# Optimization experiments

Measured on AMD Instinct MI355X. Metric: run time of the kernel, lower is better.

Reference implementation:

```python
import jax, jax.numpy as jnp
import numpy as np

N_DRUG = 20000
N_DIS = 20000
E = 300000
D_IN = 128
D_OUT = 128
W_SCALE = 0.05  # ~xavier-ish scale so leaky_relu/softmax stay well-conditioned


def setup_inputs() -> dict:
    key = jax.random.key(0)
    ks = jax.random.split(key, 17)
    f32 = jnp.float32
    inp = {
        'feat_drug': jax.random.normal(ks[0], (N_DRUG, D_IN), dtype=f32),
        'feat_disease': jax.random.normal(ks[1], (N_DIS, D_IN), dtype=f32),
        'W_ind': jax.random.normal(ks[2], (D_IN, D_OUT), dtype=f32) * W_SCALE,
        'b_ind': jax.random.normal(ks[3], (D_OUT,), dtype=f32) * W_SCALE,
        'a_ind': jax.random.normal(ks[4], (2 * D_OUT,), dtype=f32) * W_SCALE,
        'W_rev': jax.random.normal(ks[5], (D_IN, D_OUT), dtype=f32) * W_SCALE,
        'b_rev': jax.random.normal(ks[6], (D_OUT,), dtype=f32) * W_SCALE,
        'a_rev': jax.random.normal(ks[7], (2 * D_OUT,), dtype=f32) * W_SCALE,
        'W_dd': jax.random.normal(ks[8], (D_IN, D_OUT), dtype=f32) * W_SCALE,
        'b_dd': jax.random.normal(ks[9], (D_OUT,), dtype=f32) * W_SCALE,
        'a_dd': jax.random.normal(ks[10], (2 * D_OUT,), dtype=f32) * W_SCALE,
        'src_ind': jax.random.randint(ks[11], (E,), 0, N_DRUG, dtype=jnp.int32),
        'dst_ind': jax.random.randint(ks[12], (E,), 0, N_DIS, dtype=jnp.int32),
        'src_rev': jax.random.randint(ks[13], (E,), 0, N_DIS, dtype=jnp.int32),
        'dst_rev': jax.random.randint(ks[14], (E,), 0, N_DRUG, dtype=jnp.int32),
        'src_dd': jax.random.randint(ks[15], (E,), 0, N_DIS, dtype=jnp.int32),
        'dst_dd': jax.random.randint(ks[16], (E,), 0, N_DIS, dtype=jnp.int32),
    }
    return inp


def segment_softmax(e, seg, num_segments):
    # numerically stable softmax over variable-degree neighborhoods (dst segments)
    m = jax.ops.segment_max(e, seg, num_segments=num_segments)
    p = jnp.exp(e - m[seg])
    s = jax.ops.segment_sum(p, seg, num_segments=num_segments)
    return p / s[seg]


def _etype_agg(Wh_src, Wh_dst_key, a, src, dst, n_dst):
    # attn_fc(cat([Wh_src[src], Wh_dst_key[dst]])) decomposed into per-node
    # scalar projections, then gathered per edge (same math, far less traffic)
    d = Wh_src.shape[1]
    el = Wh_src @ a[:d]        # [n_src]
    er = Wh_dst_key @ a[d:]    # [n_dst]
    e = jax.nn.leaky_relu(el[src] + er[dst])          # [E], slope 0.01 as in torch
    alpha = segment_softmax(e, dst, n_dst)            # per-dst softmax (DGL mailbox)
    msg = alpha[:, None] * Wh_src[src]                # [E, d]
    return jax.ops.segment_sum(msg, dst, num_segments=n_dst)


def reference(feat_drug, feat_disease, W_ind, b_ind, a_ind, W_rev, b_rev, a_rev,
              W_dd, b_dd, a_dd, src_ind, dst_ind, src_rev, dst_rev, src_dd, dst_dd):
    # per-etype linear on source node type
    Wh_ind = feat_drug @ W_ind + b_ind       # drug nodes, etype 'indication'
    Wh_rev = feat_disease @ W_rev + b_rev    # disease nodes, etype 'rev_indication'
    Wh_dd = feat_disease @ W_dd + b_dd       # disease nodes, etype 'disease_disease'
    n_drug = feat_drug.shape[0]
    n_dis = feat_disease.shape[0]
    # etype 'indication' (drug->disease): dst key is Wh_rev_indication
    h_dis_ind = _etype_agg(Wh_ind, Wh_rev, a_ind, src_ind, dst_ind, n_dis)
    # etype 'rev_indication' (disease->drug): dst key is Wh_indication
    h_drug = _etype_agg(Wh_rev, Wh_ind, a_rev, src_rev, dst_rev, n_drug)
    # etype 'disease_disease' (homotypic): both keys Wh_dd
    h_dis_dd = _etype_agg(Wh_dd, Wh_dd, a_dd, src_dd, dst_dd, n_dis)
    # multi_update_all(..., 'sum'): sum per-etype reductions per dst node type
    h_disease = h_dis_ind + h_dis_dd
    return h_drug, h_disease
```

## Files before the change

kernel.cpp:

```cpp
#include <hip/hip_runtime.h>
#include <hip/hip_bf16.h>

typedef __hip_bfloat16 bf16;
typedef __attribute__((ext_vector_type(8))) short bf16x8;
typedef __attribute__((ext_vector_type(4))) float f32x4;

#define N_NODE 20000
#define D      128
#define NEDGE  300000
#define NROW   (3 * N_NODE)
#define NBIN   ((NROW + 255) >> 8)
#define NB3    220
#define CHUNK  4096
#define GBE    ((N_NODE + 63) / 64)
#define WT_LD  132

__device__ __forceinline__ short f2bs(float x) {
    bf16 h = __float2bfloat16(x);
    short s; __builtin_memcpy(&s, &h, 2); return s;
}

__global__ __launch_bounds__(256) void gemm_mfma_all(
    const float* __restrict__ feat_drug, const float* __restrict__ feat_dis,
    const float* __restrict__ W_ind, const float* __restrict__ b_ind,
    const float* __restrict__ a_ind,
    const float* __restrict__ W_rev, const float* __restrict__ b_rev,
    const float* __restrict__ a_rev,
    const float* __restrict__ W_dd, const float* __restrict__ b_dd,
    const float* __restrict__ a_dd,
    bf16* __restrict__ Wh_all, float* __restrict__ el_all,
    float* __restrict__ er_all) {
    __shared__ short Wt[D * WT_LD];
    const int t  = blockIdx.x / GBE;
    const int mb = blockIdx.x - t * GBE;
    const int tid = threadIdx.x;

    const float *feat, *W, *bias, *va, *vb;
    float *el_o, *er_o;
    if (t == 0)      { feat = feat_dis;  W = W_rev; bias = b_rev; va = a_rev; vb = a_ind + D; el_o = el_all;              er_o = er_all + N_NODE; }
    else if (t == 1) { feat = feat_drug; W = W_ind; bias = b_ind; va = a_ind; vb = a_rev + D; el_o = el_all + N_NODE;     er_o = er_all; }
    else             { feat = feat_dis;  W = W_dd;  bias = b_dd;  va = a_dd;  vb = a_dd + D;  el_o = el_all + 2 * N_NODE; er_o = er_all + 2 * N_NODE; }
    bf16* wh_o = Wh_all + (size_t)t * N_NODE * D;

    for (int i = tid * 4; i < D * D; i += 1024) {
        const float4 wv = *(const float4*)(W + i);
        const int k = i >> 7, n = i & (D - 1);
        Wt[(n + 0) * WT_LD + k] = f2bs(wv.x);
        Wt[(n + 1) * WT_LD + k] = f2bs(wv.y);
        Wt[(n + 2) * WT_LD + k] = f2bs(wv.z);
        Wt[(n + 3) * WT_LD + k] = f2bs(wv.w);
    }
    __syncthreads();

    const int wave = tid >> 6, lane = tid & 63;
    const int q = lane >> 4, nn = lane & 15;
    const int row0 = mb * 64 + wave * 16;
    const int arow = min(row0 + nn, N_NODE - 1);

    f32x4 acc[8];
#pragma unroll
    for (int nt = 0; nt < 8; ++nt) acc[nt] = (f32x4){0.f, 0.f, 0.f, 0.f};

#pragma unroll
    for (int ks = 0; ks < 4; ++ks) {
        const float* ap = feat + (size_t)arow * D + ks * 32 + q * 8;
        const float4 fa = *(const float4*)ap;
        const float4 fb = *(const float4*)(ap + 4);
        bf16x8 afrag;
        afrag[0] = f2bs(fa.x); afrag[1] = f2bs(fa.y);
        afrag[2] = f2bs(fa.z); afrag[3] = f2bs(fa.w);
        afrag[4] = f2bs(fb.x); afrag[5] = f2bs(fb.y);
        afrag[6] = f2bs(fb.z); afrag[7] = f2bs(fb.w);
#pragma unroll
        for (int nt = 0; nt < 8; ++nt) {
            const bf16x8 bfrag =
                *(const bf16x8*)(&Wt[(nt * 16 + nn) * WT_LD + ks * 32 + q * 8]);
            acc[nt] = __builtin_amdgcn_mfma_f32_16x16x32_bf16(afrag, bfrag,
                                                              acc[nt], 0, 0, 0);
        }
    }

    float biasv[8], vav[8], vbv[8];
#pragma unroll
    for (int nt = 0; nt < 8; ++nt) {
        const int col = nt * 16 + nn;
        biasv[nt] = bias[col]; vav[nt] = va[col]; vbv[nt] = vb[col];
    }
    float pel[4] = {0.f, 0.f, 0.f, 0.f};
    float per_[4] = {0.f, 0.f, 0.f, 0.f};
    short* whs = (short*)wh_o;
#pragma unroll
    for (int nt = 0; nt < 8; ++nt) {
#pragma unroll
        for (int r = 0; r < 4; ++r) {
            const float c = acc[nt][r] + biasv[nt];
            const int grow = row0 + q * 4 + r;
            if (grow < N_NODE)
                whs[(size_t)grow * D + nt * 16 + nn] = f2bs(c);
            pel[r] = fmaf(c, vav[nt], pel[r]);
            per_[r] = fmaf(c, vbv[nt], per_[r]);
        }
    }
#pragma unroll
    for (int r = 0; r < 4; ++r) {
#pragma unroll
        for (int mask = 1; mask < 16; mask <<= 1) {
            pel[r]  += __shfl_xor(pel[r],  mask, 64);
            per_[r] += __shfl_xor(per_[r], mask, 64);
        }
        const int grow = row0 + q * 4 + r;
        if (nn == 0 && grow < N_NODE) {
            el_o[grow] = pel[r];
            er_o[grow] = per_[r];
        }
    }
}


__global__ __launch_bounds__(256) void binct(
    const int* __restrict__ dst_rev, const int* __restrict__ dst_ind,
    const int* __restrict__ dst_dd, int* __restrict__ bin_cnt) {
    __shared__ int h[NBIN];
    const int tid = threadIdx.x;
    for (int i = tid; i < NBIN; i += 256) h[i] = 0;
    __syncthreads();
    const int base = blockIdx.x * CHUNK;
    const int lim = min(base + CHUNK, 3 * NEDGE);
    for (int i = base + tid; i < lim; i += 256) {
        const int t = (i >= 2 * NEDGE) ? 2 : (i >= NEDGE ? 1 : 0);
        const int e = i - t * NEDGE;
        const int d = (t == 0 ? dst_rev : (t == 1 ? dst_ind : dst_dd))[e];
        atomicAdd(&h[(t * N_NODE + d) >> 8], 1);
    }
    __syncthreads();
    for (int i = tid; i < NBIN; i += 256)
        if (h[i]) atomicAdd(&bin_cnt[i], h[i]);
}

__global__ __launch_bounds__(256) void binscan(
    const int* __restrict__ bin_cnt, int* __restrict__ bin_base,
    int* __restrict__ bin_cursor, int* __restrict__ row_ptr) {
    __shared__ int wsum[4];
    const int tid = threadIdx.x;
    const int lane = tid & 63, wave = tid >> 6;
    int v = (tid < NBIN) ? bin_cnt[tid] : 0;
    const int orig = v;
#pragma unroll
    for (int off = 1; off < 64; off <<= 1) {
        int t = __shfl_up(v, off, 64);
        if (lane >= off) v += t;
    }
    if (lane == 63) wsum[wave] = v;
    __syncthreads();
    if (tid == 0) {
        int a = 0;
#pragma unroll
        for (int w = 0; w < 4; ++w) { int t = wsum[w]; wsum[w] = a; a += t; }
    }
    __syncthreads();
    const int incl = wsum[wave] + v;
    const int excl = incl - orig;
    if (tid < NBIN) { bin_base[tid] = excl; bin_cursor[tid] = excl; }
    if (tid == 255) { bin_base[NBIN] = incl; row_ptr[NROW] = 3 * NEDGE; }
}

__global__ __launch_bounds__(256) void binscat(
    const int* __restrict__ src_rev, const int* __restrict__ dst_rev,
    const int* __restrict__ src_ind, const int* __restrict__ dst_ind,
    const int* __restrict__ src_dd,  const int* __restrict__ dst_dd,
    int* __restrict__ bin_cursor, unsigned* __restrict__ bin_buf) {
    __shared__ int h[NBIN];
    __shared__ int runc[NBIN];
    const int tid = threadIdx.x;
    for (int i = tid; i < NBIN; i += 256) h[i] = 0;
    __syncthreads();
    const int base = blockIdx.x * CHUNK;
    const int lim = min(base + CHUNK, 3 * NEDGE);
    for (int i = base + tid; i < lim; i += 256) {
        const int t = (i >= 2 * NEDGE) ? 2 : (i >= NEDGE ? 1 : 0);
        const int e = i - t * NEDGE;
        const int d = (t == 0 ? dst_rev : (t == 1 ? dst_ind : dst_dd))[e];
        atomicAdd(&h[(t * N_NODE + d) >> 8], 1);
    }
    __syncthreads();
    for (int i = tid; i < NBIN; i += 256)
        runc[i] = h[i] ? atomicAdd(&bin_cursor[i], h[i]) : 0;
    __syncthreads();
    for (int i = base + tid; i < lim; i += 256) {
        const int t = (i >= 2 * NEDGE) ? 2 : (i >= NEDGE ? 1 : 0);
        const int e = i - t * NEDGE;
        const int sl = (t == 0 ? src_rev : (t == 1 ? src_ind : src_dd))[e];
        const int dl = (t == 0 ? dst_rev : (t == 1 ? dst_ind : dst_dd))[e];
        const int row = t * N_NODE + dl;
        const int slot = atomicAdd(&runc[row >> 8], 1);
        bin_buf[slot] = ((unsigned)row << 16) | (unsigned)(t * N_NODE + sl);
    }
}

__global__ __launch_bounds__(256) void binsort(
    const int* __restrict__ bin_base, const unsigned* __restrict__ bin_buf,
    int* __restrict__ row_ptr, unsigned short* __restrict__ edge_src16) {
    __shared__ int rowcnt[256];
    __shared__ int rankc[256];
    __shared__ int wsum[4];
    const int b = blockIdx.x;
    const int tid = threadIdx.x;
    const int beg = bin_base[b], end = bin_base[b + 1];
    rowcnt[tid] = 0;
    __syncthreads();
    for (int i = beg + tid; i < end; i += 256)
        atomicAdd(&rowcnt[(bin_buf[i] >> 16) & 255], 1);
    __syncthreads();
    const int lane = tid & 63, wave = tid >> 6;
    int v = rowcnt[tid];
    const int orig = v;
#pragma unroll
    for (int off = 1; off < 64; off <<= 1) {
        int t = __shfl_up(v, off, 64);
        if (lane >= off) v += t;
    }
    if (lane == 63) wsum[wave] = v;
    __syncthreads();
    if (tid == 0) {
        int a = 0;
#pragma unroll
        for (int w = 0; w < 4; ++w) { int t = wsum[w]; wsum[w] = a; a += t; }
    }
    __syncthreads();
    const int excl = wsum[wave] + v - orig;
    const int row = b * 256 + tid;
    if (row < NROW) row_ptr[row] = beg + excl;
    rankc[tid] = beg + excl;
    __syncthreads();
    for (int i = beg + tid; i < end; i += 256) {
        const unsigned u = bin_buf[i];
        const int slot = atomicAdd(&rankc[(u >> 16) & 255], 1);
        edge_src16[slot] = (unsigned short)(u & 0xFFFFu);
    }
}

__device__ __forceinline__ void do_range(
    const unsigned short* __restrict__ edge_src16,
    const float* __restrict__ el_all, float er_r,
    const bf16* __restrict__ Wh_all,
    int beg, int end, int lane, float& a0, float& a1) {
    if (end <= beg) return;

    float ssum = 0.f;
    for (int base = beg; base < end; base += 64) {
        const int m = min(end - base, 64);
        if (lane < m) {
            const int sr = edge_src16[base + lane];
            float v = el_all[sr] + er_r;
            v = v > 0.f ? v : 0.01f * v;
            ssum += __expf(v);
        }
    }
#pragma unroll
    for (int off = 32; off > 0; off >>= 1) ssum += __shfl_down(ssum, off, 64);
    const float inv = 1.0f / __shfl(ssum, 0, 64);

    for (int base = beg; base < end; base += 64) {
        const int m = min(end - base, 64);
        int msrc = 0; float mpe = 0.f;
        if (lane < m) {
            msrc = edge_src16[base + lane];
            float v = el_all[msrc] + er_r;
            v = v > 0.f ? v : 0.01f * v;
            mpe = __expf(v);
        }
        int t = 0;
        for (; t + 4 <= m; t += 4) {
            const int s0 = __shfl(msrc, t,     64);
            const int s1 = __shfl(msrc, t + 1, 64);
            const int s2 = __shfl(msrc, t + 2, 64);
            const int s3 = __shfl(msrc, t + 3, 64);
            const float c0 = __shfl(mpe, t,     64) * inv;
            const float c1 = __shfl(mpe, t + 1, 64) * inv;
            const float c2 = __shfl(mpe, t + 2, 64) * inv;
            const float c3 = __shfl(mpe, t + 3, 64) * inv;
            const unsigned u0 = ((const unsigned*)(Wh_all + (size_t)s0 * D))[lane];
            const unsigned u1 = ((const unsigned*)(Wh_all + (size_t)s1 * D))[lane];
            const unsigned u2 = ((const unsigned*)(Wh_all + (size_t)s2 * D))[lane];
            const unsigned u3 = ((const unsigned*)(Wh_all + (size_t)s3 * D))[lane];
            a0 = fmaf(c0, __uint_as_float(u0 << 16), a0);
            a1 = fmaf(c0, __uint_as_float(u0 & 0xFFFF0000u), a1);
            a0 = fmaf(c1, __uint_as_float(u1 << 16), a0);
            a1 = fmaf(c1, __uint_as_float(u1 & 0xFFFF0000u), a1);
            a0 = fmaf(c2, __uint_as_float(u2 << 16), a0);
            a1 = fmaf(c2, __uint_as_float(u2 & 0xFFFF0000u), a1);
            a0 = fmaf(c3, __uint_as_float(u3 << 16), a0);
            a1 = fmaf(c3, __uint_as_float(u3 & 0xFFFF0000u), a1);
        }
        for (; t < m; ++t) {
            const int s0 = __shfl(msrc, t, 64);
            const float c0 = __shfl(mpe, t, 64) * inv;
            const unsigned u0 = ((const unsigned*)(Wh_all + (size_t)s0 * D))[lane];
            a0 = fmaf(c0, __uint_as_float(u0 << 16), a0);
            a1 = fmaf(c0, __uint_as_float(u0 & 0xFFFF0000u), a1);
        }
    }
}

__global__ __launch_bounds__(256) void gather_all(
    const int* __restrict__ row_ptr, const unsigned short* __restrict__ edge_src16,
    const float* __restrict__ el_all, const float* __restrict__ er_all,
    const bf16* __restrict__ Wh_all, float* __restrict__ out) {
    const int w = blockIdx.x * (blockDim.x >> 6) + (threadIdx.x >> 6);
    const int lane = threadIdx.x & 63;
    if (w >= 2 * N_NODE) return;

    float a0 = 0.f, a1 = 0.f;
    do_range(edge_src16, el_all, er_all[w], Wh_all,
             row_ptr[w], row_ptr[w + 1], lane, a0, a1);
    if (w >= N_NODE) {
        const int r = w + N_NODE;
        do_range(edge_src16, el_all, er_all[r], Wh_all,
                 row_ptr[r], row_ptr[r + 1], lane, a0, a1);
    }
    ((float2*)(out + (size_t)w * D))[lane] = make_float2(a0, a1);
}

extern "C" void kernel_launch(void* const* d_in, const int* in_sizes, int n_in,
                              void* d_out, int out_size, void* d_ws, size_t ws_size,
                              hipStream_t stream) {
    const float* feat_drug    = (const float*)d_in[0];
    const float* feat_disease = (const float*)d_in[1];
    const float* W_ind = (const float*)d_in[2];
    const float* b_ind = (const float*)d_in[3];
    const float* a_ind = (const float*)d_in[4];
    const float* W_rev = (const float*)d_in[5];
    const float* b_rev = (const float*)d_in[6];
    const float* a_rev = (const float*)d_in[7];
    const float* W_dd  = (const float*)d_in[8];
    const float* b_dd  = (const float*)d_in[9];
    const float* a_dd  = (const float*)d_in[10];
    const int* src_ind = (const int*)d_in[11];
    const int* dst_ind = (const int*)d_in[12];
    const int* src_rev = (const int*)d_in[13];
    const int* dst_rev = (const int*)d_in[14];
    const int* src_dd  = (const int*)d_in[15];
    const int* dst_dd  = (const int*)d_in[16];
    float* out = (float*)d_out;
    (void)in_sizes; (void)n_in; (void)out_size; (void)ws_size;

    char* w = (char*)d_ws;
    bf16*  Wh_all     = (bf16*)w;
    float* el_all     = (float*)(w + 15360000);
    float* er_all     = (float*)(w + 15600000);
    int*   row_ptr    = (int*)(w + 15840000);
    int*   bin_cnt    = (int*)(w + 16080032);
    int*   bin_base   = (int*)(w + 16081056);
    int*   bin_cursor = (int*)(w + 16082080);
    unsigned* bin_buf = (unsigned*)(w + 16083104);
    unsigned short* edge_src16 = (unsigned short*)(w + 19687584);

    const int gb = (2 * N_NODE + 3) / 4;

    gemm_mfma_all<<<3 * GBE, 256, 0, stream>>>(
        feat_drug, feat_disease, W_ind, b_ind, a_ind,
        W_rev, b_rev, a_rev, W_dd, b_dd, a_dd, Wh_all, el_all, er_all);

    hipMemsetAsync(bin_cnt, 0, NBIN * sizeof(int), stream);
    binct<<<NB3, 256, 0, stream>>>(dst_rev, dst_ind, dst_dd, bin_cnt);
    binscan<<<1, 256, 0, stream>>>(bin_cnt, bin_base, bin_cursor, row_ptr);
    binscat<<<NB3, 256, 0, stream>>>(src_rev, dst_rev, src_ind, dst_ind,
                                     src_dd, dst_dd, bin_cursor, bin_buf);
    binsort<<<NBIN, 256, 0, stream>>>(bin_base, bin_buf, row_ptr, edge_src16);

    gather_all<<<gb, 256, 0, stream>>>(row_ptr, edge_src16, el_all, er_all,
                                       Wh_all, out);
}
```

Baseline: 194.9 us.

## Fuse bin counting into GEMM launch and fold scan into scatter

```diff
diff --git a/kernel.cpp b/kernel.cpp
--- a/kernel.cpp
+++ b/kernel.cpp
@@ -13,6 +13,7 @@
 #define NB3    220
 #define CHUNK  4096
 #define GBE    ((N_NODE + 63) / 64)
+#define GEMMB  (3 * GBE)
 #define WT_LD  132
 
 __device__ __forceinline__ short f2bs(float x) {
@@ -20,7 +21,12 @@
     short s; __builtin_memcpy(&s, &h, 2); return s;
 }
 
-__global__ __launch_bounds__(256) void gemm_mfma_all(
+union SharedA {
+    short Wt[D * WT_LD];
+    int   h[NBIN];
+};
+
+__global__ __launch_bounds__(256) void gemm_and_count(
     const float* __restrict__ feat_drug, const float* __restrict__ feat_dis,
     const float* __restrict__ W_ind, const float* __restrict__ b_ind,
     const float* __restrict__ a_ind,
@@ -28,12 +34,33 @@
     const float* __restrict__ a_rev,
     const float* __restrict__ W_dd, const float* __restrict__ b_dd,
     const float* __restrict__ a_dd,
+    const int* __restrict__ dst_rev, const int* __restrict__ dst_ind,
+    const int* __restrict__ dst_dd,
     bf16* __restrict__ Wh_all, float* __restrict__ el_all,
-    float* __restrict__ er_all) {
-    __shared__ short Wt[D * WT_LD];
+    float* __restrict__ er_all, int* __restrict__ bin_part) {
+    __shared__ SharedA su;
+    const int tid = threadIdx.x;
+
+    if (blockIdx.x >= GEMMB) {
+        const int blk = blockIdx.x - GEMMB;
+        for (int i = tid; i < NBIN; i += 256) su.h[i] = 0;
+        __syncthreads();
+        const int base = blk * CHUNK;
+        const int lim = min(base + CHUNK, 3 * NEDGE);
+        for (int i = base + tid; i < lim; i += 256) {
+            const int t = (i >= 2 * NEDGE) ? 2 : (i >= NEDGE ? 1 : 0);
+            const int e = i - t * NEDGE;
+            const int d = (t == 0 ? dst_rev : (t == 1 ? dst_ind : dst_dd))[e];
+            atomicAdd(&su.h[(t * N_NODE + d) >> 8], 1);
+        }
+        __syncthreads();
+        for (int i = tid; i < NBIN; i += 256)
+            bin_part[blk * NBIN + i] = su.h[i];
+        return;
+    }
+
     const int t  = blockIdx.x / GBE;
     const int mb = blockIdx.x - t * GBE;
-    const int tid = threadIdx.x;
 
     const float *feat, *W, *bias, *va, *vb;
     float *el_o, *er_o;
@@ -45,10 +72,10 @@
     for (int i = tid * 4; i < D * D; i += 1024) {
         const float4 wv = *(const float4*)(W + i);
         const int k = i >> 7, n = i & (D - 1);
-        Wt[(n + 0) * WT_LD + k] = f2bs(wv.x);
-        Wt[(n + 1) * WT_LD + k] = f2bs(wv.y);
-        Wt[(n + 2) * WT_LD + k] = f2bs(wv.z);
-        Wt[(n + 3) * WT_LD + k] = f2bs(wv.w);
+        su.Wt[(n + 0) * WT_LD + k] = f2bs(wv.x);
+        su.Wt[(n + 1) * WT_LD + k] = f2bs(wv.y);
+        su.Wt[(n + 2) * WT_LD + k] = f2bs(wv.z);
+        su.Wt[(n + 3) * WT_LD + k] = f2bs(wv.w);
     }
     __syncthreads();
 
@@ -74,7 +101,7 @@
 #pragma unroll
         for (int nt = 0; nt < 8; ++nt) {
             const bf16x8 bfrag =
-                *(const bf16x8*)(&Wt[(nt * 16 + nn) * WT_LD + ks * 32 + q * 8]);
+                *(const bf16x8*)(&su.Wt[(nt * 16 + nn) * WT_LD + ks * 32 + q * 8]);
             acc[nt] = __builtin_amdgcn_mfma_f32_16x16x32_bf16(afrag, bfrag,
                                                               acc[nt], 0, 0, 0);
         }
@@ -116,76 +143,51 @@
     }
 }
 
-
-__global__ __launch_bounds__(256) void binct(
-    const int* __restrict__ dst_rev, const int* __restrict__ dst_ind,
-    const int* __restrict__ dst_dd, int* __restrict__ bin_cnt) {
-    __shared__ int h[NBIN];
-    const int tid = threadIdx.x;
-    for (int i = tid; i < NBIN; i += 256) h[i] = 0;
-    __syncthreads();
-    const int base = blockIdx.x * CHUNK;
-    const int lim = min(base + CHUNK, 3 * NEDGE);
-    for (int i = base + tid; i < lim; i += 256) {
-        const int t = (i >= 2 * NEDGE) ? 2 : (i >= NEDGE ? 1 : 0);
-        const int e = i - t * NEDGE;
-        const int d = (t == 0 ? dst_rev : (t == 1 ? dst_ind : dst_dd))[e];
-        atomicAdd(&h[(t * N_NODE + d) >> 8], 1);
-    }
-    __syncthreads();
-    for (int i = tid; i < NBIN; i += 256)
-        if (h[i]) atomicAdd(&bin_cnt[i], h[i]);
-}
-
-__global__ __launch_bounds__(256) void binscan(
-    const int* __restrict__ bin_cnt, int* __restrict__ bin_base,
-    int* __restrict__ bin_cursor, int* __restrict__ row_ptr) {
-    __shared__ int wsum[4];
-    const int tid = threadIdx.x;
-    const int lane = tid & 63, wave = tid >> 6;
-    int v = (tid < NBIN) ? bin_cnt[tid] : 0;
-    const int orig = v;
-#pragma unroll
-    for (int off = 1; off < 64; off <<= 1) {
-        int t = __shfl_up(v, off, 64);
-        if (lane >= off) v += t;
-    }
-    if (lane == 63) wsum[wave] = v;
-    __syncthreads();
-    if (tid == 0) {
-        int a = 0;
-#pragma unroll
-        for (int w = 0; w < 4; ++w) { int t = wsum[w]; wsum[w] = a; a += t; }
-    }
-    __syncthreads();
-    const int incl = wsum[wave] + v;
-    const int excl = incl - orig;
-    if (tid < NBIN) { bin_base[tid] = excl; bin_cursor[tid] = excl; }
-    if (tid == 255) { bin_base[NBIN] = incl; row_ptr[NROW] = 3 * NEDGE; }
-}
-
 __global__ __launch_bounds__(256) void binscat(
     const int* __restrict__ src_rev, const int* __restrict__ dst_rev,
     const int* __restrict__ src_ind, const int* __restrict__ dst_ind,
     const int* __restrict__ src_dd,  const int* __restrict__ dst_dd,
-    int* __restrict__ bin_cursor, unsigned* __restrict__ bin_buf) {
-    __shared__ int h[NBIN];
+    const int* __restrict__ bin_part, int* __restrict__ bin_base_g,
+    int* __restrict__ row_ptr, unsigned* __restrict__ bin_buf) {
     __shared__ int runc[NBIN];
+    __shared__ int wsum[4];
+    const int blk = blockIdx.x;
     const int tid = threadIdx.x;
-    for (int i = tid; i < NBIN; i += 256) h[i] = 0;
-    __syncthreads();
-    const int base = blockIdx.x * CHUNK;
+    const int lane = tid & 63, wave = tid >> 6;
+
+    int tot = 0, pre = 0;
+    if (tid < NBIN) {
+        for (int j = 0; j < NB3; ++j) {
+            const int c = bin_part[j * NBIN + tid];
+            tot += c;
+            pre += (j < blk) ? c : 0;
+        }
+    }
+    int v = (tid < NBIN) ? tot : 0;
+    const int orig = v;
+#pragma unroll
+    for (int off = 1; off < 64; off <<= 1) {
+        int t = __shfl_up(v, off, 64);
+        if (lane >= off) v += t;
+    }
+    if (lane == 63) wsum[wave] = v;
+    __syncthreads();
+    if (tid == 0) {
+        int a = 0;
+#pragma unroll
+        for (int w = 0; w < 4; ++w) { int t = wsum[w]; wsum[w] = a; a += t; }
+    }
+    __syncthreads();
+    const int excl = wsum[wave] + v - orig;
+    if (tid < NBIN) runc[tid] = excl + pre;
+    if (blk == 0) {
+        if (tid < NBIN) bin_base_g[tid] = excl;
+        if (tid == 0) { bin_base_g[NBIN] = 3 * NEDGE; row_ptr[NROW] = 3 * NEDGE; }
+    }
+    __syncthreads();
+
+    const int base = blk * CHUNK;
     const int lim = min(base + CHUNK, 3 * NEDGE);
-    for (int i = base + tid; i < lim; i += 256) {
-        const int t = (i >= 2 * NEDGE) ? 2 : (i >= NEDGE ? 1 : 0);
-        const int e = i - t * NEDGE;
-        const int d = (t == 0 ? dst_rev : (t == 1 ? dst_ind : dst_dd))[e];
-        atomicAdd(&h[(t * N_NODE + d) >> 8], 1);
-    }
-    __syncthreads();
-    for (int i = tid; i < NBIN; i += 256)
-        runc[i] = h[i] ? atomicAdd(&bin_cursor[i], h[i]) : 0;
-    __syncthreads();
     for (int i = base + tid; i < lim; i += 256) {
         const int t = (i >= 2 * NEDGE) ? 2 : (i >= NEDGE ? 1 : 0);
         const int e = i - t * NEDGE;
@@ -239,15 +241,59 @@
     }
 }
 
+__device__ __forceinline__ void process_chunk(
+    int msrc, float mpe, int m, float inv, int lane,
+    const bf16* __restrict__ Wh_all, float& a0, float& a1) {
+    int t = 0;
+    for (; t + 4 <= m; t += 4) {
+        const int s0 = __shfl(msrc, t,     64);
+        const int s1 = __shfl(msrc, t + 1, 64);
+        const int s2 = __shfl(msrc, t + 2, 64);
+        const int s3 = __shfl(msrc, t + 3, 64);
+        const float c0 = __shfl(mpe, t,     64) * inv;
+        const float c1 = __shfl(mpe, t + 1, 64) * inv;
+        const float c2 = __shfl(mpe, t + 2, 64) * inv;
+        const float c3 = __shfl(mpe, t + 3, 64) * inv;
+        const unsigned u0 = ((const unsigned*)(Wh_all + (size_t)s0 * D))[lane];
+        const unsigned u1 = ((const unsigned*)(Wh_all + (size_t)s1 * D))[lane];
+        const unsigned u2 = ((const unsigned*)(Wh_all + (size_t)s2 * D))[lane];
+        const unsigned u3 = ((const unsigned*)(Wh_all + (size_t)s3 * D))[lane];
+        a0 = fmaf(c0, __uint_as_float(u0 << 16), a0);
+        a1 = fmaf(c0, __uint_as_float(u0 & 0xFFFF0000u), a1);
+        a0 = fmaf(c1, __uint_as_float(u1 << 16), a0);
+        a1 = fmaf(c1, __uint_as_float(u1 & 0xFFFF0000u), a1);
+        a0 = fmaf(c2, __uint_as_float(u2 << 16), a0);
+        a1 = fmaf(c2, __uint_as_float(u2 & 0xFFFF0000u), a1);
+        a0 = fmaf(c3, __uint_as_float(u3 << 16), a0);
+        a1 = fmaf(c3, __uint_as_float(u3 & 0xFFFF0000u), a1);
+    }
+    for (; t < m; ++t) {
+        const int s0 = __shfl(msrc, t, 64);
+        const float c0 = __shfl(mpe, t, 64) * inv;
+        const unsigned u0 = ((const unsigned*)(Wh_all + (size_t)s0 * D))[lane];
+        a0 = fmaf(c0, __uint_as_float(u0 << 16), a0);
+        a1 = fmaf(c0, __uint_as_float(u0 & 0xFFFF0000u), a1);
+    }
+}
+
 __device__ __forceinline__ void do_range(
     const unsigned short* __restrict__ edge_src16,
     const float* __restrict__ el_all, float er_r,
     const bf16* __restrict__ Wh_all,
     int beg, int end, int lane, float& a0, float& a1) {
     if (end <= beg) return;
-
-    float ssum = 0.f;
-    for (int base = beg; base < end; base += 64) {
+    const int deg = end - beg;
+    const int m0 = min(deg, 64);
+
+    int msrc0 = 0; float mpe0 = 0.f;
+    if (lane < m0) {
+        msrc0 = edge_src16[beg + lane];
+        float v = el_all[msrc0] + er_r;
+        v = v > 0.f ? v : 0.01f * v;
+        mpe0 = __expf(v);
+    }
+    float ssum = mpe0;
+    for (int base = beg + 64; base < end; base += 64) {
         const int m = min(end - base, 64);
         if (lane < m) {
             const int sr = edge_src16[base + lane];
@@ -260,7 +306,8 @@
     for (int off = 32; off > 0; off >>= 1) ssum += __shfl_down(ssum, off, 64);
     const float inv = 1.0f / __shfl(ssum, 0, 64);
 
-    for (int base = beg; base < end; base += 64) {
+    process_chunk(msrc0, mpe0, m0, inv, lane, Wh_all, a0, a1);
+    for (int base = beg + 64; base < end; base += 64) {
         const int m = min(end - base, 64);
         int msrc = 0; float mpe = 0.f;
         if (lane < m) {
@@ -269,36 +316,7 @@
             v = v > 0.f ? v : 0.01f * v;
             mpe = __expf(v);
         }
-        int t = 0;
-        for (; t + 4 <= m; t += 4) {
-            const int s0 = __shfl(msrc, t,     64);
-            const int s1 = __shfl(msrc, t + 1, 64);
-            const int s2 = __shfl(msrc, t + 2, 64);
-            const int s3 = __shfl(msrc, t + 3, 64);
-            const float c0 = __shfl(mpe, t,     64) * inv;
-            const float c1 = __shfl(mpe, t + 1, 64) * inv;
-            const float c2 = __shfl(mpe, t + 2, 64) * inv;
-            const float c3 = __shfl(mpe, t + 3, 64) * inv;
-            const unsigned u0 = ((const unsigned*)(Wh_all + (size_t)s0 * D))[lane];
-            const unsigned u1 = ((const unsigned*)(Wh_all + (size_t)s1 * D))[lane];
-            const unsigned u2 = ((const unsigned*)(Wh_all + (size_t)s2 * D))[lane];
-            const unsigned u3 = ((const unsigned*)(Wh_all + (size_t)s3 * D))[lane];
-            a0 = fmaf(c0, __uint_as_float(u0 << 16), a0);
-            a1 = fmaf(c0, __uint_as_float(u0 & 0xFFFF0000u), a1);
-            a0 = fmaf(c1, __uint_as_float(u1 << 16), a0);
-            a1 = fmaf(c1, __uint_as_float(u1 & 0xFFFF0000u), a1);
-            a0 = fmaf(c2, __uint_as_float(u2 << 16), a0);
-            a1 = fmaf(c2, __uint_as_float(u2 & 0xFFFF0000u), a1);
-            a0 = fmaf(c3, __uint_as_float(u3 << 16), a0);
-            a1 = fmaf(c3, __uint_as_float(u3 & 0xFFFF0000u), a1);
-        }
-        for (; t < m; ++t) {
-            const int s0 = __shfl(msrc, t, 64);
-            const float c0 = __shfl(mpe, t, 64) * inv;
-            const unsigned u0 = ((const unsigned*)(Wh_all + (size_t)s0 * D))[lane];
-            a0 = fmaf(c0, __uint_as_float(u0 << 16), a0);
-            a1 = fmaf(c0, __uint_as_float(u0 & 0xFFFF0000u), a1);
-        }
+        process_chunk(msrc, mpe, m, inv, lane, Wh_all, a0, a1);
     }
 }
 
@@ -345,27 +363,26 @@
     (void)in_sizes; (void)n_in; (void)out_size; (void)ws_size;
 
     char* w = (char*)d_ws;
-    bf16*  Wh_all     = (bf16*)w;
-    float* el_all     = (float*)(w + 15360000);
-    float* er_all     = (float*)(w + 15600000);
-    int*   row_ptr    = (int*)(w + 15840000);
-    int*   bin_cnt    = (int*)(w + 16080032);
-    int*   bin_base   = (int*)(w + 16081056);
-    int*   bin_cursor = (int*)(w + 16082080);
-    unsigned* bin_buf = (unsigned*)(w + 16083104);
-    unsigned short* edge_src16 = (unsigned short*)(w + 19687584);
+    bf16*  Wh_all   = (bf16*)w;
+    float* el_all   = (float*)(w + 15360000);
+    float* er_all   = (float*)(w + 15600000);
+    int*   row_ptr  = (int*)(w + 15840000);
+    int*   bin_base = (int*)(w + 16080032);
+    int*   bin_part = (int*)(w + 16081056);
+    unsigned* bin_buf = (unsigned*)(w + 16287872);
+    unsigned short* edge_src16 = (unsigned short*)(w + 19887872);
 
     const int gb = (2 * N_NODE + 3) / 4;
 
-    gemm_mfma_all<<<3 * GBE, 256, 0, stream>>>(
+    gemm_and_count<<<GEMMB + NB3, 256, 0, stream>>>(
         feat_drug, feat_disease, W_ind, b_ind, a_ind,
-        W_rev, b_rev, a_rev, W_dd, b_dd, a_dd, Wh_all, el_all, er_all);
-
-    hipMemsetAsync(bin_cnt, 0, NBIN * sizeof(int), stream);
-    binct<<<NB3, 256, 0, stream>>>(dst_rev, dst_ind, dst_dd, bin_cnt);
-    binscan<<<1, 256, 0, stream>>>(bin_cnt, bin_base, bin_cursor, row_ptr);
+        W_rev, b_rev, a_rev, W_dd, b_dd, a_dd,
+        dst_rev, dst_ind, dst_dd, Wh_all, el_all, er_all, bin_part);
+
     binscat<<<NB3, 256, 0, stream>>>(src_rev, dst_rev, src_ind, dst_ind,
-                                     src_dd, dst_dd, bin_cursor, bin_buf);
+                                     src_dd, dst_dd, bin_part, bin_base,
+                                     row_ptr, bin_buf);
+
     binsort<<<NBIN, 256, 0, stream>>>(bin_base, bin_buf, row_ptr, edge_src16);
 
     gather_all<<<gb, 256, 0, stream>>>(row_ptr, edge_src16, el_all, er_all,
```

After: 181.3 us. 1.07x faster.
